# Performance work log

Measured on AMD Instinct MI355X. Metric: run time of the kernel, lower is better.

Reference implementation:

```python
import jax, jax.numpy as jnp
import numpy as np

# constants from VMD_block.__init__ (K=4, alpha=2000, tau=0, DC=0, init=1, tol=5e-5, max_N=5)
K = 4
ALPHA = 2000.0
TAU = 0.0
TOL = 5e-05
MAX_N = 5


def _mvmd(f):
    """Multivariate VMD (Rehman & Aftab 2019) on f: (C, T) real signals.
    Returns modes u: (K, C, T). Shared center frequencies omega across channels."""
    C, T = f.shape
    half = T // 2
    T2 = 2 * T
    # mirror extension to length 2T
    fM = jnp.concatenate([f[:, :half][:, ::-1], f, f[:, half:][:, ::-1]], axis=1)
    freqs = (jnp.arange(1, T2 + 1, dtype=f.dtype) / T2) - 0.5 - (1.0 / T2)  # (T2,)
    f_hat = jnp.fft.fftshift(jnp.fft.fft(fM, axis=1), axes=1).astype(jnp.complex64)
    h2 = T2 // 2
    f_hat_plus = f_hat.at[:, :h2].set(0.0)  # keep analytic (positive-freq) part
    fpos = freqs[h2:]

    omega0 = (0.5 / K) * jnp.arange(K, dtype=f.dtype)  # init == 1, DC == 0
    u0 = jnp.zeros((K, C, T2), dtype=jnp.complex64)
    lam0 = jnp.zeros((C, T2), dtype=jnp.complex64)

    def cond(st):
        _, _, _, n, uDiff = st
        return jnp.logical_and(uDiff > TOL, n < MAX_N)

    def body(st):
        u, omega, lam, n, _ = st
        u_prev = u
        sum_all = jnp.sum(u, axis=0)  # (C, T2)
        for k in range(K):  # Gauss-Seidel mode updates; K is small & static
            sum_uk = sum_all - u[k]
            denom = 1.0 + ALPHA * (freqs - omega[k]) ** 2  # (T2,)
            u_k = (f_hat_plus - sum_uk - lam / 2.0) / denom
            sum_all = sum_uk + u_k
            u = u.at[k].set(u_k)
            power = jnp.abs(u_k[:, h2:]) ** 2  # (C, T2/2) positive freqs
            omega = omega.at[k].set(jnp.sum(fpos * power) / jnp.sum(power))
        lam = lam + TAU * (sum_all - f_hat_plus)  # tau == 0 -> dual ascent is a no-op
        d = u - u_prev
        uDiff = jnp.abs(jnp.sum(d * jnp.conj(d)) / T2) + jnp.finfo(jnp.float32).eps
        return u, omega, lam, n + 1, uDiff.astype(jnp.float32)

    st0 = (u0, omega0, lam0, jnp.int32(0), jnp.float32(TOL + 1.0))
    u, omega, lam, n, uDiff = jax.lax.while_loop(cond, body, st0)

    # rebuild full spectrum via Hermitian symmetry, back to time domain
    u_hat = jnp.zeros((K, C, T2), dtype=jnp.complex64)
    u_hat = u_hat.at[:, :, h2:].set(u[:, :, h2:])
    u_hat = u_hat.at[:, :, 1:h2 + 1].set(jnp.conj(u[:, :, h2:])[:, :, ::-1])
    u_hat = u_hat.at[:, :, 0].set(jnp.conj(u_hat[:, :, -1]))
    ut = jnp.real(jnp.fft.ifft(jnp.fft.ifftshift(u_hat, axes=-1), axis=-1))
    return ut[:, :, T2 // 4: 3 * T2 // 4]  # crop mirror padding -> (K, C, T)


def setup_inputs() -> dict:
    key = jax.random.key(0)
    x = jax.random.normal(key, (8, 2048, 64), dtype=jnp.float32)  # (B, T, C)
    return {"x": x}


def reference(x):
    B, T, C = x.shape
    xr = jnp.transpose(x, (0, 2, 1)).reshape(B * C, T)  # (B*C, T)
    u = _mvmd(xr)  # (K, B*C, T)
    x_l = jnp.transpose(u[0].reshape(B, C, T), (0, 2, 1))  # lowest-freq mode -> (B, T, C)
    x_h = x - x_l
    return (x_h, x_l)
```

## Files before the change

### kernel.cpp

```cpp
#include <hip/hip_runtime.h>
#include <math.h>

#define TLEN 2048
#define T2   4096
#define H2   2048
#define NBLK 512
#define EPS32 1.1920928955078125e-07

__device__ __forceinline__ double ld_acc(const double* p){
  return __hip_atomic_load(p, __ATOMIC_RELAXED, __HIP_MEMORY_SCOPE_AGENT);
}

__device__ __forceinline__ void gbar(unsigned* bar){
  __syncthreads();
  if (threadIdx.x == 0){
    __hip_atomic_fetch_add(bar, 1u, __ATOMIC_RELAXED, __HIP_MEMORY_SCOPE_AGENT);
    unsigned spins = 0;
    while (__hip_atomic_load(bar, __ATOMIC_RELAXED, __HIP_MEMORY_SCOPE_AGENT) < NBLK){
      if (++spins > (1u << 20)) break;
      __builtin_amdgcn_s_sleep(8);
    }
  }
  __syncthreads();
}

__device__ __forceinline__ void r4_stages(float2* src, float2* dst,
                                          const float2* twl, float sgn, int nst){
  const int tid = threadIdx.x;
  #pragma unroll 1
  for (int t = 0; t < nst; ++t){
    const int L = 2 << (2 * t);
    const int Lm = L - 1;
    #pragma unroll
    for (int bf = 0; bf < 2; ++bf){
      int idx = tid + (bf << 8);
      int q  = idx & Lm;
      int tb = idx - q;
      float2 a = src[idx];
      float2 b = src[idx + 512];
      float2 c = src[idx + 1024];
      float2 d = src[idx + 1536];
      float2 w1 = twl[2 * tb];
      float2 w2 = twl[4 * tb];
      float2 w3 = twl[6 * tb];
      float w1y = sgn * w1.y, w2y = sgn * w2.y, w3y = sgn * w3.y;
      float t0x = a.x + c.x, t0y = a.y + c.y;
      float t1x = a.x - c.x, t1y = a.y - c.y;
      float t2x = b.x + d.x, t2y = b.y + d.y;
      float t3x = sgn * (b.y - d.y);
      float t3y = -sgn * (b.x - d.x);
      float y0x = t0x + t2x, y0y = t0y + t2y;
      float y1x = t1x + t3x, y1y = t1y + t3y;
      float y2x = t0x - t2x, y2y = t0y - t2y;
      float y3x = t1x - t3x, y3y = t1y - t3y;
      int ob = q + (tb << 2);
      dst[ob]         = make_float2(y0x, y0y);
      dst[ob + L]     = make_float2(y1x * w1.x - y1y * w1y, y1x * w1y + y1y * w1.x);
      dst[ob + 2 * L] = make_float2(y2x * w2.x - y2y * w2y, y2x * w2y + y2y * w2.x);
      dst[ob + 3 * L] = make_float2(y3x * w3.x - y3y * w3y, y3x * w3y + y3y * w3.x);
    }
    __syncthreads();
    float2* tt = src; src = dst; dst = tt;
  }
}

__device__ __forceinline__ double wred(double v){
  #pragma unroll
  for (int off = 32; off; off >>= 1) v += __shfl_down(v, off);
  return v;
}

__device__ __forceinline__ void red9(double a0, double a1, double a2, double a3,
                                     double a4, double a5, double a6, double a7,
                                     double a8, double* red, double* accs){
  const int tid = threadIdx.x, wave = tid >> 6, lane = tid & 63;
  double r;
  r = wred(a0); if (lane == 0) red[ 0 + wave] = r;
  r = wred(a1); if (lane == 0) red[ 4 + wave] = r;
  r = wred(a2); if (lane == 0) red[ 8 + wave] = r;
  r = wred(a3); if (lane == 0) red[12 + wave] = r;
  r = wred(a4); if (lane == 0) red[16 + wave] = r;
  r = wred(a5); if (lane == 0) red[20 + wave] = r;
  r = wred(a6); if (lane == 0) red[24 + wave] = r;
  r = wred(a7); if (lane == 0) red[28 + wave] = r;
  r = wred(a8); if (lane == 0) red[32 + wave] = r;
  __syncthreads();
  if (tid < 9)
    atomicAdd(&accs[tid], red[tid*4+0] + red[tid*4+1] + red[tid*4+2] + red[tid*4+3]);
}

#define MODE_S(UXc, UYc, OMc, AFP, AP) {                       \
  float ox_ = sx - (UXc), oy_ = sy - (UYc);                    \
  float d_  = fj - (OMc);                                      \
  float den_ = 1.0f + 2000.0f * d_ * d_;                       \
  float nx_ = (Fx - ox_) / den_, ny_ = (Fy - oy_) / den_;      \
  float pw_ = nx_ * nx_ + ny_ * ny_;                           \
  AFP += (double)(fj * pw_);  AP += (double)pw_;               \
  float ddx_ = nx_ - (UXc), ddy_ = ny_ - (UYc);                \
  aD += (double)(ddx_ * ddx_ + ddy_ * ddy_);                   \
  (UXc) = nx_; (UYc) = ny_;                                    \
  sx = ox_ + nx_; sy = oy_ + ny_; }

#define BIN_S(PP, UX, UY) {                                    \
  int j = tid + ((PP) << 8);                                   \
  float2 Fv = bufB[j];                                         \
  float Fx = Fv.x, Fy = Fv.y;                                  \
  float fj = (float)j * (1.0f / 4096.0f);                      \
  float sx = UX.x + UX.y + UX.z + UX.w;                        \
  float sy = UY.x + UY.y + UY.z + UY.w;                        \
  MODE_S(UX.x, UY.x, om.x, aFP0, aP0)                          \
  MODE_S(UX.y, UY.y, om.y, aFP1, aP1)                          \
  MODE_S(UX.z, UY.z, om.z, aFP2, aP2)                          \
  MODE_S(UX.w, UY.w, om.w, aFP3, aP3) }

#define IT1(PP, UX, UY) { UX = make_float4(0.f,0.f,0.f,0.f);   \
                          UY = make_float4(0.f,0.f,0.f,0.f);   \
                          BIN_S(PP, UX, UY) }

#define HERMU(PP, UX, UY) {                                    \
  int j = tid + ((PP) << 8);                                   \
  float vx, vy;                                                \
  if (act){                                                    \
    float2 Fv = bufB[j];                                       \
    float sx = UX.y + UX.z + UX.w;                             \
    float sy = UY.y + UY.z + UY.w;                             \
    float fj = (float)j * (1.0f / 4096.0f);                    \
    float dd = fj - om0;                                       \
    float den = 1.0f + 2000.0f * dd * dd;                      \
    vx = (Fv.x - sx) / den; vy = (Fv.y - sy) / den;            \
  } else { vx = UX.x; vy = UY.x; }                             \
  bufA[j] = make_float2(vx, vy); }

#define FOR8(M) M(0,ux0,uy0) M(1,ux1,uy1) M(2,ux2,uy2) M(3,ux3,uy3) \
                M(4,ux4,uy4) M(5,ux5,uy5) M(6,ux6,uy6) M(7,ux7,uy7)

#define R2F(BF, ZA, ZB) {                                      \
  int p = tid + ((BF) << 8);                                   \
  float2 w = twl[2 * p];                                       \
  float dx = ZA.x - ZB.x, dy = ZA.y - ZB.y;                    \
  *reinterpret_cast<float4*>(&bufB[2 * p]) =                   \
    make_float4(ZA.x + ZB.x, ZA.y + ZB.y,                      \
                dx * w.x - dy * w.y, dx * w.y + dy * w.x); }

#define ILAST(IDX, Y1, Y2) {                                   \
  float2 a = bufA[IDX];                                        \
  float2 bb = bufA[(IDX) + 512];                               \
  float2 c = bufA[(IDX) + 1024];                               \
  float2 d = bufA[(IDX) + 1536];                               \
  float t1x = a.x - c.x, t1y = a.y - c.y;                      \
  float t3x = -(bb.y - d.y), t3y = (bb.x - d.x);               \
  Y1 = make_float2(t1x + t3x, t1y + t3y);                      \
  float t0x = a.x + c.x, t0y = a.y + c.y;                      \
  float t2x = bb.x + d.x, t2y = bb.y + d.y;                    \
  Y2 = make_float2(t0x - t2x, t0y - t2y); }

__global__ void k_boot(float2* __restrict__ tw, unsigned* __restrict__ syncz){
  int p = blockIdx.x * 256 + threadIdx.x;
  double a = -6.283185307179586 * (double)p / 4096.0;
  tw[p] = make_float2((float)cos(a), (float)sin(a));
  if (blockIdx.x == 0 && threadIdx.x < 128) syncz[threadIdx.x] = 0u;
}

__global__ void __attribute__((amdgpu_flat_work_group_size(256, 256),
                               amdgpu_waves_per_eu(2, 2)))
k_main(const float* __restrict__ x, const float2* __restrict__ tw,
       unsigned* __restrict__ bar, double* __restrict__ accs,
       float* __restrict__ xh, float* __restrict__ xl){
  __shared__ float2 twl[3072];
  __shared__ float2 bufA[H2];
  __shared__ float2 bufB[H2];
  __shared__ float somf[8];
  const int tid = threadIdx.x;
  const int b = blockIdx.x & 7, ch = blockIdx.x >> 3;
  const float* xc = x + (size_t)b * TLEN * 64 + ch;

  #pragma unroll
  for (int i = 0; i < 12; ++i)
    twl[tid + (i << 8)] = tw[tid + (i << 8)];

  float2 z0, z1, z2, z3, z4, z5, z6, z7;
  z0 = make_float2(xc[(size_t)(1023 - 2*tid) * 64], xc[(size_t)(1022 - 2*tid) * 64]);
  z1 = make_float2(xc[(size_t)( 511 - 2*tid) * 64], xc[(size_t)( 510 - 2*tid) * 64]);
  { int t = 2*tid;        z2 = make_float2(xc[(size_t)t*64], xc[(size_t)(t+1)*64]); }
  { int t = 2*tid + 512;  z3 = make_float2(xc[(size_t)t*64], xc[(size_t)(t+1)*64]); }
  { int t = 2*tid + 1024; z4 = make_float2(xc[(size_t)t*64], xc[(size_t)(t+1)*64]); }
  { int t = 2*tid + 1536; z5 = make_float2(xc[(size_t)t*64], xc[(size_t)(t+1)*64]); }
  z6 = make_float2(xc[(size_t)(2047 - 2*tid) * 64], xc[(size_t)(2046 - 2*tid) * 64]);
  z7 = make_float2(xc[(size_t)(1535 - 2*tid) * 64], xc[(size_t)(1534 - 2*tid) * 64]);
  __syncthreads();

  R2F(0, z0, z4)  R2F(1, z1, z5)  R2F(2, z2, z6)  R2F(3, z3, z7)
  __syncthreads();
  r4_stages(bufB, bufA, twl, 1.0f, 5);

  #pragma unroll
  for (int pp = 0; pp < 8; ++pp){
    int k = tid + (pp << 8);
    float2 A  = bufA[k];
    float2 Zm = bufA[(2048 - k) & 2047];
    float px = 0.5f * (A.x + Zm.x), py = 0.5f * (A.y - Zm.y);
    float qx = 0.5f * (A.x - Zm.x), qy = 0.5f * (A.y + Zm.y);
    float2 W = twl[k];
    bufB[k] = make_float2(px + W.x * qy + W.y * qx,
                          py - W.x * qx + W.y * qy);
  }
  __syncthreads();

  float4 ux0, ux1, ux2, ux3, ux4, ux5, ux6, ux7;
  float4 uy0, uy1, uy2, uy3, uy4, uy5, uy6, uy7;
  float4 om = make_float4(0.0f, 0.125f, 0.25f, 0.375f);

  {
    double aFP0=0,aFP1=0,aFP2=0,aFP3=0,aP0=0,aP1=0,aP2=0,aP3=0,aD=0;
    FOR8(IT1)
    red9(aFP0,aFP1,aFP2,aFP3,aP0,aP1,aP2,aP3,aD, (double*)bufA, accs);
  }

  bool active = true;
  double* slot = accs;
  #pragma unroll 1
  for (int it = 0; it < 3; ++it){
    gbar(bar + it);
    if (tid < 4) somf[tid] = (float)(ld_acc(slot + tid) / ld_acc(slot + 4 + tid));
    if (tid == 7) somf[7] = (ld_acc(slot + 8) * (1.0/4096.0) + EPS32 > 5e-5) ? 1.f : 0.f;
    __syncthreads();
    if (active){
      if (somf[7] != 0.0f){
        om.x = somf[0]; om.y = somf[1]; om.z = somf[2]; om.w = somf[3];
      } else active = false;
    }
    if (active){
      double aFP0=0,aFP1=0,aFP2=0,aFP3=0,aP0=0,aP1=0,aP2=0,aP3=0,aD=0;
      FOR8(BIN_S)
      red9(aFP0,aFP1,aFP2,aFP3,aP0,aP1,aP2,aP3,aD, (double*)bufA, slot + 9);
    }
    slot += 9;
  }
  gbar(bar + 3);

  if (tid == 0) somf[0] = (float)(ld_acc(slot) / ld_acc(slot + 4));
  if (tid == 7) somf[7] = (ld_acc(slot + 8) * (1.0/4096.0) + EPS32 > 5e-5) ? 1.f : 0.f;
  __syncthreads();
  {
    bool act = active && (somf[7] != 0.0f);
    float om0 = somf[0];
    FOR8(HERMU)
    __syncthreads();
    #pragma unroll
    for (int pp = 0; pp < 8; ++pp){
      int k = tid + (pp << 8);
      float2 Zv;
      if (k == 0){
        float e = bufA[0].x + bufA[2047].x;
        float o = bufA[0].x - bufA[2047].x;
        Zv = make_float2(e, o);
      } else {
        float2 A  = bufA[k];
        float2 Bm = bufA[2048 - k];
        float ex = A.x + Bm.x, ey = A.y - Bm.y;
        float dx = A.x - Bm.x, dy = A.y + Bm.y;
        float2 W = twl[k];
        float ox = dx * W.x + dy * W.y;
        float oy = dy * W.x - dx * W.y;
        Zv = make_float2(ex - oy, ey + ox);
      }
      bufB[k] = Zv;
    }
    __syncthreads();
    #pragma unroll
    for (int bf = 0; bf < 4; ++bf){
      int p = tid + (bf << 8);
      float2 a = bufB[p], bb = bufB[p + 1024];
      float2 w = twl[2 * p];
      float dx = a.x - bb.x, dy = a.y - bb.y;
      *reinterpret_cast<float4*>(&bufA[2 * p]) =
        make_float4(a.x + bb.x, a.y + bb.y,
                    dx * w.x + dy * w.y, -dx * w.y + dy * w.x);
    }
    __syncthreads();
    r4_stages(bufA, bufB, twl, -1.0f, 4);
  }

  {
    const float scale = 1.0f / 4096.0f;
    float2 y1a, y2a, y1b, y2b;
    ILAST(tid,       y1a, y2a)
    ILAST(tid + 256, y1b, y2b)
    #define STOUT(YV, T0, ZS) {                                \
      size_t o0 = ((size_t)(b * TLEN + (T0))) * 64 + ch;       \
      float l0 = YV.x * scale, l1 = YV.y * scale;              \
      xh[o0]      = ZS.x - l0;  xl[o0]      = l0;              \
      xh[o0 + 64] = ZS.y - l1;  xl[o0 + 64] = l1; }
    STOUT(y1a, 2*tid,        z2)
    STOUT(y1b, 2*tid + 512,  z3)
    STOUT(y2a, 2*tid + 1024, z4)
    STOUT(y2b, 2*tid + 1536, z5)
  }
}

extern "C" void kernel_launch(void* const* d_in, const int* in_sizes, int n_in,
                              void* d_out, int out_size, void* d_ws, size_t ws_size,
                              hipStream_t stream){
  const float* x = (const float*)d_in[0];
  float* out_xh = (float*)d_out;
  float* out_xl = out_xh + (size_t)8 * TLEN * 64;

  char* ws = (char*)d_ws;
  float2* tw   = (float2*)ws;
  char*   sync = ws + 32768;
  unsigned* bar  = (unsigned*)sync;
  double*   accs = (double*)(sync + 128);

  k_boot<<<12, 256, 0, stream>>>(tw, (unsigned*)sync);
  k_main<<<NBLK, 256, 0, stream>>>(x, tw, bar, accs, out_xh, out_xl);
}
```

Measured before the change: 137.2 us.

## Fuse first FFT stages in registers and keep spectrum bins in registers

Merges the initial radix-2 stage and the first radix-4 stage of the forward and inverse FFTs into a register-resident butterfly (fused2), which removes one shared-memory pass and one barrier per FFT. The real-to-complex post-processing result is kept in registers (f0..f7) instead of being written to bufB and reread every VMD iteration. The inverse pre-processing is also computed into registers before the fused stage, and a dedicated shared reduction buffer replaces reuse of bufA. This raises register pressure while the kernel is pinned at two waves per EU, so spilling is a risk.

```diff
diff --git a/kernel.cpp b/kernel.cpp
--- a/kernel.cpp
+++ b/kernel.cpp
@@ -24,12 +24,54 @@
   __syncthreads();
 }
 
+#define R2REG(ZA, ZB, W, SGN, E, O) {                           \
+  float wy_ = (SGN) * W.y;                                      \
+  E = make_float2(ZA.x + ZB.x, ZA.y + ZB.y);                    \
+  float dx_ = ZA.x - ZB.x, dy_ = ZA.y - ZB.y;                   \
+  O = make_float2(dx_ * W.x - dy_ * wy_, dx_ * wy_ + dy_ * W.x); }
+
+#define R4REG(A, B, C, D, W1, W2, W3, SGN, Y0, Y1, Y2, Y3) {    \
+  float w1y_ = (SGN)*W1.y, w2y_ = (SGN)*W2.y, w3y_ = (SGN)*W3.y;\
+  float t0x = A.x + C.x, t0y = A.y + C.y;                       \
+  float t1x = A.x - C.x, t1y = A.y - C.y;                       \
+  float t2x = B.x + D.x, t2y = B.y + D.y;                       \
+  float t3x = (SGN) * (B.y - D.y), t3y = -(SGN) * (B.x - D.x);  \
+  Y0 = make_float2(t0x + t2x, t0y + t2y);                       \
+  float y1x = t1x + t3x, y1y = t1y + t3y;                       \
+  float y2x = t0x - t2x, y2y = t0y - t2y;                       \
+  float y3x = t1x - t3x, y3y = t1y - t3y;                       \
+  Y1 = make_float2(y1x*W1.x - y1y*w1y_, y1x*w1y_ + y1y*W1.x);   \
+  Y2 = make_float2(y2x*W2.x - y2y*w2y_, y2x*w2y_ + y2y*W2.x);   \
+  Y3 = make_float2(y3x*W3.x - y3y*w3y_, y3x*w3y_ + y3y*W3.x); }
+
+__device__ __forceinline__ void fused2(float2 z0, float2 z1, float2 z2, float2 z3,
+                                       float2 z4, float2 z5, float2 z6, float2 z7,
+                                       const float2* twl, float sgn, float2* dst){
+  const int tid = threadIdx.x;
+  float2 wa = twl[2*tid], wb = twl[2*tid+512], wc = twl[2*tid+1024], wd = twl[2*tid+1536];
+  float2 e0,o0,e1,o1,e2,o2,e3,o3;
+  R2REG(z0, z4, wa, sgn, e0, o0)
+  R2REG(z1, z5, wb, sgn, e1, o1)
+  R2REG(z2, z6, wc, sgn, e2, o2)
+  R2REG(z3, z7, wd, sgn, e3, o3)
+  float2 w1 = twl[4*tid], w2 = twl[8*tid], w3 = twl[12*tid];
+  float2 a0,a1,a2,a3, b0,b1,b2,b3;
+  R4REG(e0, e1, e2, e3, w1, w2, w3, sgn, a0, a1, a2, a3)
+  R4REG(o0, o1, o2, o3, w1, w2, w3, sgn, b0, b1, b2, b3)
+  float4* d4 = reinterpret_cast<float4*>(dst + 8 * tid);
+  d4[0] = make_float4(a0.x, a0.y, b0.x, b0.y);
+  d4[1] = make_float4(a1.x, a1.y, b1.x, b1.y);
+  d4[2] = make_float4(a2.x, a2.y, b2.x, b2.y);
+  d4[3] = make_float4(a3.x, a3.y, b3.x, b3.y);
+}
+
 __device__ __forceinline__ void r4_stages(float2* src, float2* dst,
-                                          const float2* twl, float sgn, int nst){
+                                          const float2* twl, float sgn,
+                                          int first, int cnt){
   const int tid = threadIdx.x;
   #pragma unroll 1
-  for (int t = 0; t < nst; ++t){
-    const int L = 2 << (2 * t);
+  for (int t = 0; t < cnt; ++t){
+    const int L = 2 << (2 * (first + t));
     const int Lm = L - 1;
     #pragma unroll
     for (int bf = 0; bf < 2; ++bf){
@@ -43,21 +85,13 @@
       float2 w1 = twl[2 * tb];
       float2 w2 = twl[4 * tb];
       float2 w3 = twl[6 * tb];
-      float w1y = sgn * w1.y, w2y = sgn * w2.y, w3y = sgn * w3.y;
-      float t0x = a.x + c.x, t0y = a.y + c.y;
-      float t1x = a.x - c.x, t1y = a.y - c.y;
-      float t2x = b.x + d.x, t2y = b.y + d.y;
-      float t3x = sgn * (b.y - d.y);
-      float t3y = -sgn * (b.x - d.x);
-      float y0x = t0x + t2x, y0y = t0y + t2y;
-      float y1x = t1x + t3x, y1y = t1y + t3y;
-      float y2x = t0x - t2x, y2y = t0y - t2y;
-      float y3x = t1x - t3x, y3y = t1y - t3y;
+      float2 y0, y1, y2, y3;
+      R4REG(a, b, c, d, w1, w2, w3, sgn, y0, y1, y2, y3)
       int ob = q + (tb << 2);
-      dst[ob]         = make_float2(y0x, y0y);
-      dst[ob + L]     = make_float2(y1x * w1.x - y1y * w1y, y1x * w1y + y1y * w1.x);
-      dst[ob + 2 * L] = make_float2(y2x * w2.x - y2y * w2y, y2x * w2y + y2y * w2.x);
-      dst[ob + 3 * L] = make_float2(y3x * w3.x - y3y * w3y, y3x * w3y + y3y * w3.x);
+      dst[ob]         = y0;
+      dst[ob + L]     = y1;
+      dst[ob + 2 * L] = y2;
+      dst[ob + 3 * L] = y3;
     }
     __syncthreads();
     float2* tt = src; src = dst; dst = tt;
@@ -101,11 +135,9 @@
   (UXc) = nx_; (UYc) = ny_;                                    \
   sx = ox_ + nx_; sy = oy_ + ny_; }
 
-#define BIN_S(PP, UX, UY) {                                    \
-  int j = tid + ((PP) << 8);                                   \
-  float2 Fv = bufB[j];                                         \
-  float Fx = Fv.x, Fy = Fv.y;                                  \
-  float fj = (float)j * (1.0f / 4096.0f);                      \
+#define BIN_S(PP, FV, UX, UY) {                                \
+  float Fx = FV.x, Fy = FV.y;                                  \
+  float fj = (float)(tid + ((PP) << 8)) * (1.0f / 4096.0f);    \
   float sx = UX.x + UX.y + UX.z + UX.w;                        \
   float sy = UY.x + UY.y + UY.z + UY.w;                        \
   MODE_S(UX.x, UY.x, om.x, aFP0, aP0)                          \
@@ -113,34 +145,52 @@
   MODE_S(UX.z, UY.z, om.z, aFP2, aP2)                          \
   MODE_S(UX.w, UY.w, om.w, aFP3, aP3) }
 
-#define IT1(PP, UX, UY) { UX = make_float4(0.f,0.f,0.f,0.f);   \
-                          UY = make_float4(0.f,0.f,0.f,0.f);   \
-                          BIN_S(PP, UX, UY) }
-
-#define HERMU(PP, UX, UY) {                                    \
+#define IT1(PP, FV, UX, UY) { UX = make_float4(0.f,0.f,0.f,0.f); \
+                              UY = make_float4(0.f,0.f,0.f,0.f); \
+                              BIN_S(PP, FV, UX, UY) }
+
+#define FCOMP(PP, FV) {                                        \
+  int k = tid + ((PP) << 8);                                   \
+  float2 A  = bufA[k];                                         \
+  float2 Zm = bufA[(2048 - k) & 2047];                         \
+  float px = 0.5f * (A.x + Zm.x), py = 0.5f * (A.y - Zm.y);    \
+  float qx = 0.5f * (A.x - Zm.x), qy = 0.5f * (A.y + Zm.y);    \
+  float2 W = twl[k];                                           \
+  FV = make_float2(px + W.x * qy + W.y * qx,                   \
+                   py - W.x * qx + W.y * qy); }
+
+#define HERMU(PP, FV, UX, UY) {                                \
   int j = tid + ((PP) << 8);                                   \
   float vx, vy;                                                \
   if (act){                                                    \
-    float2 Fv = bufB[j];                                       \
     float sx = UX.y + UX.z + UX.w;                             \
     float sy = UY.y + UY.z + UY.w;                             \
     float fj = (float)j * (1.0f / 4096.0f);                    \
     float dd = fj - om0;                                       \
     float den = 1.0f + 2000.0f * dd * dd;                      \
-    vx = (Fv.x - sx) / den; vy = (Fv.y - sy) / den;            \
+    vx = (FV.x - sx) / den; vy = (FV.y - sy) / den;            \
   } else { vx = UX.x; vy = UY.x; }                             \
   bufA[j] = make_float2(vx, vy); }
 
-#define FOR8(M) M(0,ux0,uy0) M(1,ux1,uy1) M(2,ux2,uy2) M(3,ux3,uy3) \
-                M(4,ux4,uy4) M(5,ux5,uy5) M(6,ux6,uy6) M(7,ux7,uy7)
-
-#define R2F(BF, ZA, ZB) {                                      \
-  int p = tid + ((BF) << 8);                                   \
-  float2 w = twl[2 * p];                                       \
-  float dx = ZA.x - ZB.x, dy = ZA.y - ZB.y;                    \
-  *reinterpret_cast<float4*>(&bufB[2 * p]) =                   \
-    make_float4(ZA.x + ZB.x, ZA.y + ZB.y,                      \
-                dx * w.x - dy * w.y, dx * w.y + dy * w.x); }
+#define ZPCOMP(PP, ZV) {                                       \
+  int k = tid + ((PP) << 8);                                   \
+  if (k == 0){                                                 \
+    float e = bufA[0].x + bufA[2047].x;                        \
+    float o = bufA[0].x - bufA[2047].x;                        \
+    ZV = make_float2(e, o);                                    \
+  } else {                                                     \
+    float2 A  = bufA[k];                                       \
+    float2 Bm = bufA[2048 - k];                                \
+    float ex = A.x + Bm.x, ey = A.y - Bm.y;                    \
+    float dx = A.x - Bm.x, dy = A.y + Bm.y;                    \
+    float2 W = twl[k];                                         \
+    float ox = dx * W.x + dy * W.y;                            \
+    float oy = dy * W.x - dx * W.y;                            \
+    ZV = make_float2(ex - oy, ey + ox);                        \
+  } }
+
+#define FOR8F(M) M(0,f0,ux0,uy0) M(1,f1,ux1,uy1) M(2,f2,ux2,uy2) M(3,f3,ux3,uy3) \
+                 M(4,f4,ux4,uy4) M(5,f5,ux5,uy5) M(6,f6,ux6,uy6) M(7,f7,ux7,uy7)
 
 #define ILAST(IDX, Y1, Y2) {                                   \
   float2 a = bufA[IDX];                                        \
@@ -169,6 +219,7 @@
   __shared__ float2 twl[3072];
   __shared__ float2 bufA[H2];
   __shared__ float2 bufB[H2];
+  __shared__ double red[36];
   __shared__ float somf[8];
   const int tid = threadIdx.x;
   const int b = blockIdx.x & 7, ch = blockIdx.x >> 3;
@@ -189,22 +240,13 @@
   z7 = make_float2(xc[(size_t)(1535 - 2*tid) * 64], xc[(size_t)(1534 - 2*tid) * 64]);
   __syncthreads();
 
-  R2F(0, z0, z4)  R2F(1, z1, z5)  R2F(2, z2, z6)  R2F(3, z3, z7)
-  __syncthreads();
-  r4_stages(bufB, bufA, twl, 1.0f, 5);
-
-  #pragma unroll
-  for (int pp = 0; pp < 8; ++pp){
-    int k = tid + (pp << 8);
-    float2 A  = bufA[k];
-    float2 Zm = bufA[(2048 - k) & 2047];
-    float px = 0.5f * (A.x + Zm.x), py = 0.5f * (A.y - Zm.y);
-    float qx = 0.5f * (A.x - Zm.x), qy = 0.5f * (A.y + Zm.y);
-    float2 W = twl[k];
-    bufB[k] = make_float2(px + W.x * qy + W.y * qx,
-                          py - W.x * qx + W.y * qy);
-  }
-  __syncthreads();
+  fused2(z0, z1, z2, z3, z4, z5, z6, z7, twl, 1.0f, bufA);
+  __syncthreads();
+  r4_stages(bufA, bufB, twl, 1.0f, 1, 4);
+
+  float2 f0, f1, f2, f3, f4, f5, f6, f7;
+  FCOMP(0, f0) FCOMP(1, f1) FCOMP(2, f2) FCOMP(3, f3)
+  FCOMP(4, f4) FCOMP(5, f5) FCOMP(6, f6) FCOMP(7, f7)
 
   float4 ux0, ux1, ux2, ux3, ux4, ux5, ux6, ux7;
   float4 uy0, uy1, uy2, uy3, uy4, uy5, uy6, uy7;
@@ -212,8 +254,8 @@
 
   {
     double aFP0=0,aFP1=0,aFP2=0,aFP3=0,aP0=0,aP1=0,aP2=0,aP3=0,aD=0;
-    FOR8(IT1)
-    red9(aFP0,aFP1,aFP2,aFP3,aP0,aP1,aP2,aP3,aD, (double*)bufA, accs);
+    FOR8F(IT1)
+    red9(aFP0,aFP1,aFP2,aFP3,aP0,aP1,aP2,aP3,aD, red, accs);
   }
 
   bool active = true;
@@ -231,54 +273,28 @@
     }
     if (active){
       double aFP0=0,aFP1=0,aFP2=0,aFP3=0,aP0=0,aP1=0,aP2=0,aP3=0,aD=0;
-      FOR8(BIN_S)
-      red9(aFP0,aFP1,aFP2,aFP3,aP0,aP1,aP2,aP3,aD, (double*)bufA, slot + 9);
+      FOR8F(BIN_S)
+      red9(aFP0,aFP1,aFP2,aFP3,aP0,aP1,aP2,aP3,aD, red, slot + 9);
     }
     slot += 9;
   }
   gbar(bar + 3);
-
   if (tid == 0) somf[0] = (float)(ld_acc(slot) / ld_acc(slot + 4));
   if (tid == 7) somf[7] = (ld_acc(slot + 8) * (1.0/4096.0) + EPS32 > 5e-5) ? 1.f : 0.f;
   __syncthreads();
+
   {
     bool act = active && (somf[7] != 0.0f);
     float om0 = somf[0];
-    FOR8(HERMU)
-    __syncthreads();
-    #pragma unroll
-    for (int pp = 0; pp < 8; ++pp){
-      int k = tid + (pp << 8);
-      float2 Zv;
-      if (k == 0){
-        float e = bufA[0].x + bufA[2047].x;
-        float o = bufA[0].x - bufA[2047].x;
-        Zv = make_float2(e, o);
-      } else {
-        float2 A  = bufA[k];
-        float2 Bm = bufA[2048 - k];
-        float ex = A.x + Bm.x, ey = A.y - Bm.y;
-        float dx = A.x - Bm.x, dy = A.y + Bm.y;
-        float2 W = twl[k];
-        float ox = dx * W.x + dy * W.y;
-        float oy = dy * W.x - dx * W.y;
-        Zv = make_float2(ex - oy, ey + ox);
-      }
-      bufB[k] = Zv;
-    }
-    __syncthreads();
-    #pragma unroll
-    for (int bf = 0; bf < 4; ++bf){
-      int p = tid + (bf << 8);
-      float2 a = bufB[p], bb = bufB[p + 1024];
-      float2 w = twl[2 * p];
-      float dx = a.x - bb.x, dy = a.y - bb.y;
-      *reinterpret_cast<float4*>(&bufA[2 * p]) =
-        make_float4(a.x + bb.x, a.y + bb.y,
-                    dx * w.x + dy * w.y, -dx * w.y + dy * w.x);
-    }
-    __syncthreads();
-    r4_stages(bufA, bufB, twl, -1.0f, 4);
+    FOR8F(HERMU)
+    __syncthreads();
+    float2 p0, p1, p2, p3, p4, p5, p6, p7;
+    ZPCOMP(0, p0) ZPCOMP(1, p1) ZPCOMP(2, p2) ZPCOMP(3, p3)
+    ZPCOMP(4, p4) ZPCOMP(5, p5) ZPCOMP(6, p6) ZPCOMP(7, p7)
+    __syncthreads();
+    fused2(p0, p1, p2, p3, p4, p5, p6, p7, twl, -1.0f, bufB);
+    __syncthreads();
+    r4_stages(bufB, bufA, twl, -1.0f, 1, 3);
   }
 
   {
@@ -306,10 +322,10 @@
   float* out_xl = out_xh + (size_t)8 * TLEN * 64;
 
   char* ws = (char*)d_ws;
-  float2* tw   = (float2*)ws;
-  char*   sync = ws + 32768;
-  unsigned* bar  = (unsigned*)sync;
-  double*   accs = (double*)(sync + 128);
+  float2* tw    = (float2*)ws;
+  char*   sync  = ws + 32768;
+  unsigned* bar = (unsigned*)sync;
+  double* accs  = (double*)(sync + 128);
 
   k_boot<<<12, 256, 0, stream>>>(tw, (unsigned*)sync);
   k_main<<<NBLK, 256, 0, stream>>>(x, tw, bar, accs, out_xh, out_xl);
```

After: 135.4 us. About the same (-1.4%).
